# Performance work log

Measured on AMD Instinct MI355X. Metric: run time of the kernel, lower is better.

## Reference

```python
import jax, jax.numpy as jnp
import numpy as np

K = 10           # polynomial order
N = 100000       # num nodes
E = 3200000      # num edges
F_IN = 512       # input feature dim
C = 64           # num classes


def setup_inputs() -> dict:
    key = jax.random.key(0)
    ks = jax.random.split(key, 6)
    x = jax.random.normal(ks[0], (N, F_IN), dtype=jnp.float32)
    edge_index = jax.random.randint(ks[1], (2, E), 0, N, dtype=jnp.int64)
    W = jax.random.normal(ks[2], (F_IN, C), dtype=jnp.float32) * (1.0 / np.sqrt(F_IN))
    b = jax.random.normal(ks[3], (C,), dtype=jnp.float32) * 0.01
    lap_coefs = jax.random.uniform(ks[4], (K + 1,), dtype=jnp.float32)
    mf_weights = jax.random.uniform(ks[5], (1, K + 1, C), dtype=jnp.float32)
    return {"x": x, "edge_index": edge_index, "W": W, "b": b,
            "lap_coefs": lap_coefs, "mf_weights": mf_weights}


def reference(x, edge_index, W, b, lap_coefs, mf_weights):
    row, col = edge_index[0], edge_index[1]
    # GCN norm without self-loops: deg over targets (col), sym normalization
    ones = jnp.ones((row.shape[0],), dtype=x.dtype)
    deg = jax.ops.segment_sum(ones, col, num_segments=N)
    dinv = jnp.where(deg > 0, jax.lax.rsqrt(jnp.maximum(deg, 1.0)), 1.0)
    norm = dinv[row] * dinv[col]  # [E]

    h = x @ W + b  # [N, C]  (dropout is identity in eval mode)

    def prop(hx):
        # out[i] = sum_{(j->i)} norm_e * hx[j]
        return jax.ops.segment_sum(norm[:, None] * hx[row], col, num_segments=N)

    outs = [h, prop(h)]
    for _ in range(2, K + 1):
        # P_n = Bn*P_{n-1} + Cn*P_{n-2} + An*prop(P_{n-1}), An=2, Bn=0, Cn=-1
        outs.append(2.0 * prop(outs[-1]) - outs[-2])

    # coef_upd='none' -> coefs used directly; P0 gets coef 1, P_i gets lap_coefs[i-1]
    coefs = jnp.concatenate([jnp.ones((1,), lap_coefs.dtype), lap_coefs[:K]])  # [K+1]
    stacked = jnp.stack(outs, axis=1)  # [N, K+1, C]
    ret = jnp.sum(stacked * coefs[None, :, None] * mf_weights, axis=1)  # [N, C]
    return jax.nn.log_softmax(ret, axis=-1)
```

## Files before the change

kernel.cpp:

```cpp
#include <hip/hip_runtime.h>

#define F_IN 512
#define C_DIM 64
#define BUCKET_BITS 9
#define EPB 2048

typedef __bf16 bf16x8 __attribute__((ext_vector_type(8)));
typedef float f32x4 __attribute__((ext_vector_type(4)));

__device__ inline unsigned bf_rne(float x) {
    unsigned u = __float_as_uint(x);
    u += 0x7fffu + ((u >> 16) & 1u);
    return u >> 16;
}
__device__ inline unsigned bfpack(float x, float y) {
    return bf_rne(x) | (bf_rne(y) << 16);
}
__device__ inline bf16x8 as_bf16x8(uint4 u) {
    bf16x8 v; __builtin_memcpy(&v, &u, 16); return v;
}

__global__ void deg_kernel(const int* __restrict__ col, int* __restrict__ deg, int E) {
    int i = blockIdx.x * blockDim.x + threadIdx.x;
    int e = i * 4;
    if (e + 3 < E) {
        int4 c4 = *(const int4*)(col + e);
        atomicAdd(&deg[c4.x], 1);
        atomicAdd(&deg[c4.y], 1);
        atomicAdd(&deg[c4.z], 1);
        atomicAdd(&deg[c4.w], 1);
    } else if (e < E) {
        for (int j = e; j < E; ++j) atomicAdd(&deg[col[j]], 1);
    }
}

__global__ void dinv_kernel(const int* __restrict__ deg, float* __restrict__ dinv, int N) {
    int i = blockIdx.x * blockDim.x + threadIdx.x;
    if (i < N) {
        int d = deg[i];
        dinv[i] = (d > 0) ? (1.0f / sqrtf((float)d)) : 1.0f;
    }
}

__global__ void scan1(const int* __restrict__ deg, int* __restrict__ rowptr,
                      int* __restrict__ bsum, int N) {
    __shared__ int tmp[1024];
    int t = threadIdx.x;
    int gid = blockIdx.x * 1024 + t;
    int v = (gid < N) ? deg[gid] : 0;
    tmp[t] = v;
    __syncthreads();
    for (int off = 1; off < 1024; off <<= 1) {
        int u = (t >= off) ? tmp[t - off] : 0;
        __syncthreads();
        tmp[t] += u;
        __syncthreads();
    }
    if (gid < N) rowptr[gid] = tmp[t] - v;
    if (t == 1023) bsum[blockIdx.x] = tmp[1023];
}

__global__ void scan2(int* __restrict__ bs, int nb) {
    __shared__ int tmp[1024];
    int t = threadIdx.x;
    int v = (t < nb) ? bs[t] : 0;
    tmp[t] = v;
    __syncthreads();
    for (int off = 1; off < 1024; off <<= 1) {
        int u = (t >= off) ? tmp[t - off] : 0;
        __syncthreads();
        tmp[t] += u;
        __syncthreads();
    }
    if (t < nb) bs[t] = tmp[t] - v;
}

__global__ void scan3(int* __restrict__ rowptr, const int* __restrict__ bs, int E, int N) {
    int gid = blockIdx.x * 1024 + threadIdx.x;
    if (gid < N) rowptr[gid] += bs[blockIdx.x];
    if (gid == 0) rowptr[N] = E;
}

__global__ void bucketptr_kernel(const int* __restrict__ rowptr, int* __restrict__ bucketptr,
                                 int N, int NB) {
    int b = blockIdx.x * blockDim.x + threadIdx.x;
    if (b <= NB) {
        int idx = b << BUCKET_BITS;
        if (idx > N) idx = N;
        bucketptr[b] = rowptr[idx];
    }
}

__global__ void bucket_scatter(const int* __restrict__ row, const int* __restrict__ col,
                               const float* __restrict__ dinv,
                               const int* __restrict__ bucketptr, int* __restrict__ bcnt,
                               int2* __restrict__ staged, int* __restrict__ staged_dst, int E) {
    __shared__ int lcnt[256];
    __shared__ int lbase[256];
    int t = threadIdx.x;
    lcnt[t] = 0;
    __syncthreads();
    int base_e = blockIdx.x * EPB;
    int rr[8], cc[8], pk[8];
    #pragma unroll
    for (int j = 0; j < 8; ++j) {
        int e = base_e + j * 256 + t;
        pk[j] = -1;
        if (e < E) {
            rr[j] = row[e];
            cc[j] = col[e];
            int b = cc[j] >> BUCKET_BITS;
            int off = atomicAdd(&lcnt[b], 1);
            pk[j] = off | (b << 20);
        }
    }
    __syncthreads();
    lbase[t] = atomicAdd(&bcnt[t], lcnt[t]);
    __syncthreads();
    #pragma unroll
    for (int j = 0; j < 8; ++j) {
        if (pk[j] >= 0) {
            int b = pk[j] >> 20;
            int off = pk[j] & 0xFFFFF;
            int pos = bucketptr[b] + lbase[b] + off;
            staged[pos] = make_int2(rr[j], __float_as_int(dinv[rr[j]] * dinv[cc[j]]));
            staged_dst[pos] = cc[j];
        }
    }
}

__global__ void final_scatter(const int2* __restrict__ staged, const int* __restrict__ staged_dst,
                              const int* __restrict__ rowptr, int* __restrict__ cnt,
                              int2* __restrict__ edges, int E) {
    int i = blockIdx.x * blockDim.x + threadIdx.x;
    if (i >= E) return;
    int c = staged_dst[i];
    int pos = rowptr[c] + atomicAdd(&cnt[c], 1);
    edges[pos] = staged[i];
}

__global__ void wprep_kernel(const float* __restrict__ W,
                             uint4* __restrict__ whi, uint4* __restrict__ wlo) {
    int tid = blockIdx.x * 256 + threadIdx.x;
    int kslot = tid >> 8;
    int rem = tid & 255;
    int ct = rem >> 6;
    int l = rem & 63;
    int col = ct * 16 + (l & 15);
    int kbase = kslot * 32 + ((l >> 4) << 3);
    unsigned hbits[8], lbits[8];
    #pragma unroll
    for (int j = 0; j < 8; ++j) {
        float f = W[(size_t)(kbase + j) * C_DIM + col];
        unsigned h = bf_rne(f);
        hbits[j] = h;
        lbits[j] = bf_rne(f - __uint_as_float(h << 16));
    }
    whi[tid] = make_uint4(hbits[0] | (hbits[1] << 16), hbits[2] | (hbits[3] << 16),
                          hbits[4] | (hbits[5] << 16), hbits[6] | (hbits[7] << 16));
    wlo[tid] = make_uint4(lbits[0] | (lbits[1] << 16), lbits[2] | (lbits[3] << 16),
                          lbits[4] | (lbits[5] << 16), lbits[6] | (lbits[7] << 16));
}

__global__ __launch_bounds__(256) void gemm_mfma(const float4* __restrict__ x4,
                                                 const uint4* __restrict__ whi,
                                                 const uint4* __restrict__ wlo,
                                                 const float* __restrict__ bias,
                                                 uint4* __restrict__ hb, int N) {
    __shared__ float smem[8704];
    char* ahi = (char*)smem;
    char* alo = ahi + 16384;
    const int t = threadIdx.x;
    const int l = t & 63;
    const int wv = t >> 6;
    const int rowblk = blockIdx.x * 128;

    f32x4 acc[2][4];
    #pragma unroll
    for (int rt = 0; rt < 2; ++rt)
        #pragma unroll
        for (int ct = 0; ct < 4; ++ct) acc[rt][ct] = (f32x4){0.f, 0.f, 0.f, 0.f};

    for (int chunk = 0; chunk < 8; ++chunk) {
        #pragma unroll
        for (int i = 0; i < 4; ++i) {
            int idx = t + 256 * i;
            int r = idx >> 3, g = idx & 7;
            int grow = rowblk + r;
            float4 v0 = make_float4(0.f, 0.f, 0.f, 0.f), v1 = v0;
            if (grow < N) {
                const float4* p = x4 + (size_t)grow * (F_IN / 4) + chunk * 16 + g * 2;
                v0 = p[0]; v1 = p[1];
            }
            float f[8] = {v0.x, v0.y, v0.z, v0.w, v1.x, v1.y, v1.z, v1.w};
            unsigned hbits[8], lbits[8];
            #pragma unroll
            for (int j = 0; j < 8; ++j) {
                unsigned h = bf_rne(f[j]);
                hbits[j] = h;
                lbits[j] = bf_rne(f[j] - __uint_as_float(h << 16));
            }
            int off = r * 128 + ((g ^ (r & 7)) << 4);
            *(uint4*)(ahi + off) = make_uint4(hbits[0] | (hbits[1] << 16), hbits[2] | (hbits[3] << 16),
                                              hbits[4] | (hbits[5] << 16), hbits[6] | (hbits[7] << 16));
            *(uint4*)(alo + off) = make_uint4(lbits[0] | (lbits[1] << 16), lbits[2] | (lbits[3] << 16),
                                              lbits[4] | (lbits[5] << 16), lbits[6] | (lbits[7] << 16));
        }
        __syncthreads();
        uint4 AH[2][2], AL[2][2];
        #pragma unroll
        for (int rt = 0; rt < 2; ++rt) {
            int r = wv * 32 + rt * 16 + (l & 15);
            int rb = r * 128;
            int rx = r & 7;
            #pragma unroll
            for (int ks = 0; ks < 2; ++ks) {
                int gl = ks * 4 + (l >> 4);
                int off = rb + ((gl ^ rx) << 4);
                AH[rt][ks] = *(const uint4*)(ahi + off);
                AL[rt][ks] = *(const uint4*)(alo + off);
            }
        }
        #pragma unroll
        for (int ct = 0; ct < 4; ++ct) {
            int base = (chunk * 8 + ct) * 64 + l;
            uint4 BH0 = whi[base], BH1 = whi[base + 256];
            uint4 BL0 = wlo[base], BL1 = wlo[base + 256];
            #pragma unroll
            for (int rt = 0; rt < 2; ++rt) {
                f32x4 c = acc[rt][ct];
                c = __builtin_amdgcn_mfma_f32_16x16x32_bf16(as_bf16x8(AH[rt][0]), as_bf16x8(BH0), c, 0, 0, 0);
                c = __builtin_amdgcn_mfma_f32_16x16x32_bf16(as_bf16x8(AH[rt][1]), as_bf16x8(BH1), c, 0, 0, 0);
                c = __builtin_amdgcn_mfma_f32_16x16x32_bf16(as_bf16x8(AL[rt][0]), as_bf16x8(BH0), c, 0, 0, 0);
                c = __builtin_amdgcn_mfma_f32_16x16x32_bf16(as_bf16x8(AL[rt][1]), as_bf16x8(BH1), c, 0, 0, 0);
                c = __builtin_amdgcn_mfma_f32_16x16x32_bf16(as_bf16x8(AH[rt][0]), as_bf16x8(BL0), c, 0, 0, 0);
                c = __builtin_amdgcn_mfma_f32_16x16x32_bf16(as_bf16x8(AH[rt][1]), as_bf16x8(BL1), c, 0, 0, 0);
                acc[rt][ct] = c;
            }
        }
        __syncthreads();
    }
    float* ls = smem;
    #pragma unroll
    for (int rt = 0; rt < 2; ++rt) {
        int rbase = wv * 32 + rt * 16 + ((l >> 4) << 2);
        #pragma unroll
        for (int ct = 0; ct < 4; ++ct) {
            int col = ct * 16 + (l & 15);
            float bb = bias[col];
            #pragma unroll
            for (int q = 0; q < 4; ++q)
                ls[(rbase + q) * 68 + col] = acc[rt][ct][q] + bb;
        }
    }
    __syncthreads();
    #pragma unroll
    for (int i = 0; i < 4; ++i) {
        int idx = t + 256 * i;
        int r = idx >> 3, lc = idx & 7;
        int grow = rowblk + r;
        if (grow < N) {
            const float* p = ls + r * 68 + lc * 8;
            float4 A = *(const float4*)p;
            float4 Bv = *(const float4*)(p + 4);
            uint4 nb;
            nb.x = bfpack(A.x, A.y);
            nb.y = bfpack(A.z, A.w);
            nb.z = bfpack(Bv.x, Bv.y);
            nb.w = bfpack(Bv.z, Bv.w);
            hb[(size_t)grow * 8 + lc] = nb;
        }
    }
}

__global__ void prop_kernel(const int* __restrict__ rowptr, const int2* __restrict__ edges,
                            const uint4* __restrict__ Hb, const uint4* Pold,
                            uint4* Pout, float4* ret, const float* lap,
                            const float4* mf4, int k, int mode, int N) {
    int gtid = blockIdx.x * blockDim.x + threadIdx.x;
    int node = gtid >> 3;
    int lc = gtid & 7;
    if (node >= N) return;
    int beg = rowptr[node];
    int end = rowptr[node + 1];
    float a0 = 0.f, a1 = 0.f, a2 = 0.f, a3 = 0.f, a4 = 0.f, a5 = 0.f, a6 = 0.f, a7 = 0.f;

#define EDGE_FMA(SRC, WB) do { \
        float w_ = __int_as_float(WB); \
        uint4 u_ = Hb[(size_t)(SRC) * 8 + lc]; \
        a0 = fmaf(w_, __uint_as_float(u_.x << 16), a0); \
        a1 = fmaf(w_, __uint_as_float(u_.x & 0xffff0000u), a1); \
        a2 = fmaf(w_, __uint_as_float(u_.y << 16), a2); \
        a3 = fmaf(w_, __uint_as_float(u_.y & 0xffff0000u), a3); \
        a4 = fmaf(w_, __uint_as_float(u_.z << 16), a4); \
        a5 = fmaf(w_, __uint_as_float(u_.z & 0xffff0000u), a5); \
        a6 = fmaf(w_, __uint_as_float(u_.w << 16), a6); \
        a7 = fmaf(w_, __uint_as_float(u_.w & 0xffff0000u), a7); \
    } while (0)

    int e = beg;
    if ((e & 1) && e < end) {
        int2 d = edges[e];
        EDGE_FMA(d.x, d.y);
        ++e;
    }
    for (; e + 4 <= end; e += 4) {
        int4 p0v = ((const int4*)edges)[e >> 1];
        int4 p1v = ((const int4*)edges)[(e >> 1) + 1];
        EDGE_FMA(p0v.x, p0v.y);
        EDGE_FMA(p0v.z, p0v.w);
        EDGE_FMA(p1v.x, p1v.y);
        EDGE_FMA(p1v.z, p1v.w);
    }
    for (; e < end; ++e) {
        int2 d = edges[e];
        EDGE_FMA(d.x, d.y);
    }
#undef EDGE_FMA

    size_t ib = (size_t)node * 8 + lc;
    float p0, p1, p2, p3, p4, p5, p6, p7;
    if (mode == 0) {
        p0 = a0; p1 = a1; p2 = a2; p3 = a3; p4 = a4; p5 = a5; p6 = a6; p7 = a7;
    } else {
        uint4 ob = Pold[ib];
        p0 = 2.f * a0 - __uint_as_float(ob.x << 16);
        p1 = 2.f * a1 - __uint_as_float(ob.x & 0xffff0000u);
        p2 = 2.f * a2 - __uint_as_float(ob.y << 16);
        p3 = 2.f * a3 - __uint_as_float(ob.y & 0xffff0000u);
        p4 = 2.f * a4 - __uint_as_float(ob.z << 16);
        p5 = 2.f * a5 - __uint_as_float(ob.z & 0xffff0000u);
        p6 = 2.f * a6 - __uint_as_float(ob.w << 16);
        p7 = 2.f * a7 - __uint_as_float(ob.w & 0xffff0000u);
    }
    uint4 nb;
    nb.x = bfpack(p0, p1);
    nb.y = bfpack(p2, p3);
    nb.z = bfpack(p4, p5);
    nb.w = bfpack(p6, p7);
    Pout[ib] = nb;

    if (ret) {
        float lw = lap[k - 1];
        size_t i16 = (size_t)node * 16 + lc * 2;
        float4 m0 = mf4[k * 16 + lc * 2];
        float4 m1 = mf4[k * 16 + lc * 2 + 1];
        float4 r0 = ret[i16];
        float4 r1 = ret[i16 + 1];
        r0.x = fmaf(lw * m0.x, p0, r0.x);
        r0.y = fmaf(lw * m0.y, p1, r0.y);
        r0.z = fmaf(lw * m0.z, p2, r0.z);
        r0.w = fmaf(lw * m0.w, p3, r0.w);
        r1.x = fmaf(lw * m1.x, p4, r1.x);
        r1.y = fmaf(lw * m1.y, p5, r1.y);
        r1.z = fmaf(lw * m1.z, p6, r1.z);
        r1.w = fmaf(lw * m1.w, p7, r1.w);
        ret[i16] = r0;
        ret[i16 + 1] = r1;
    }
}

__global__ void combine_kernel(const uint4* __restrict__ hb, const uint4* __restrict__ Pall,
                               const float* __restrict__ lap, const float* __restrict__ mf,
                               float4* __restrict__ ret, int Kp, int N) {
    __shared__ float smf[1024];
    __shared__ float slap[32];
    int t = threadIdx.x;
    int nmf = (Kp + 1) * 64;
    for (int i = t; i < nmf; i += 256) smf[i] = mf[i];
    if (t < Kp) slap[t] = lap[t];
    __syncthreads();
    int g = blockIdx.x * 256 + t;
    int node = g >> 3, lc = g & 7;
    if (node >= N) return;
    size_t off = (size_t)node * 8 + lc;
    uint4 u = hb[off];
    const float* m0 = smf + lc * 8;
    float a0 = __uint_as_float(u.x << 16) * m0[0];
    float a1 = __uint_as_float(u.x & 0xffff0000u) * m0[1];
    float a2 = __uint_as_float(u.y << 16) * m0[2];
    float a3 = __uint_as_float(u.y & 0xffff0000u) * m0[3];
    float a4 = __uint_as_float(u.z << 16) * m0[4];
    float a5 = __uint_as_float(u.z & 0xffff0000u) * m0[5];
    float a6 = __uint_as_float(u.w << 16) * m0[6];
    float a7 = __uint_as_float(u.w & 0xffff0000u) * m0[7];
    size_t stride = (size_t)N * 8;
    for (int k = 1; k <= Kp; ++k) {
        uint4 p = Pall[(size_t)(k - 1) * stride + off];
        float cw = slap[k - 1];
        const float* mk = smf + k * 64 + lc * 8;
        a0 = fmaf(cw * mk[0], __uint_as_float(p.x << 16), a0);
        a1 = fmaf(cw * mk[1], __uint_as_float(p.x & 0xffff0000u), a1);
        a2 = fmaf(cw * mk[2], __uint_as_float(p.y << 16), a2);
        a3 = fmaf(cw * mk[3], __uint_as_float(p.y & 0xffff0000u), a3);
        a4 = fmaf(cw * mk[4], __uint_as_float(p.z << 16), a4);
        a5 = fmaf(cw * mk[5], __uint_as_float(p.z & 0xffff0000u), a5);
        a6 = fmaf(cw * mk[6], __uint_as_float(p.w << 16), a6);
        a7 = fmaf(cw * mk[7], __uint_as_float(p.w & 0xffff0000u), a7);
    }
    float m = fmaxf(fmaxf(fmaxf(a0, a1), fmaxf(a2, a3)), fmaxf(fmaxf(a4, a5), fmaxf(a6, a7)));
    for (int o = 1; o < 8; o <<= 1) m = fmaxf(m, __shfl_xor(m, o, 8));
    float s = __expf(a0 - m) + __expf(a1 - m) + __expf(a2 - m) + __expf(a3 - m)
            + __expf(a4 - m) + __expf(a5 - m) + __expf(a6 - m) + __expf(a7 - m);
    for (int o = 1; o < 8; o <<= 1) s += __shfl_xor(s, o, 8);
    float lg = logf(s) + m;
    ret[(size_t)node * 16 + lc * 2]     = make_float4(a0 - lg, a1 - lg, a2 - lg, a3 - lg);
    ret[(size_t)node * 16 + lc * 2 + 1] = make_float4(a4 - lg, a5 - lg, a6 - lg, a7 - lg);
}

__global__ void p0ret_kernel(const uint4* __restrict__ hb, float4* __restrict__ ret,
                             const float4* __restrict__ mf4, int N) {
    int g = blockIdx.x * 256 + threadIdx.x;
    int node = g >> 3, lc = g & 7;
    if (node >= N) return;
    uint4 u = hb[(size_t)node * 8 + lc];
    float4 m0 = mf4[lc * 2], m1 = mf4[lc * 2 + 1];
    float4 r0 = make_float4(__uint_as_float(u.x << 16) * m0.x,
                            __uint_as_float(u.x & 0xffff0000u) * m0.y,
                            __uint_as_float(u.y << 16) * m0.z,
                            __uint_as_float(u.y & 0xffff0000u) * m0.w);
    float4 r1 = make_float4(__uint_as_float(u.z << 16) * m1.x,
                            __uint_as_float(u.z & 0xffff0000u) * m1.y,
                            __uint_as_float(u.w << 16) * m1.z,
                            __uint_as_float(u.w & 0xffff0000u) * m1.w);
    ret[(size_t)node * 16 + lc * 2] = r0;
    ret[(size_t)node * 16 + lc * 2 + 1] = r1;
}

__global__ void lsm_kernel(float* __restrict__ ret, int N) {
    int wid = (blockIdx.x * blockDim.x + threadIdx.x) >> 6;
    int c = threadIdx.x & 63;
    if (wid >= N) return;
    size_t idx = (size_t)wid * C_DIM + c;
    float v = ret[idx];
    float m = v;
    for (int off = 32; off; off >>= 1) m = fmaxf(m, __shfl_xor(m, off, 64));
    float ex = __expf(v - m);
    float s = ex;
    for (int off = 32; off; off >>= 1) s += __shfl_xor(s, off, 64);
    ret[idx] = (v - m) - logf(s);
}

extern "C" void kernel_launch(void* const* d_in, const int* in_sizes, int n_in,
                              void* d_out, int out_size, void* d_ws, size_t ws_size,
                              hipStream_t stream) {
    const float* x   = (const float*)d_in[0];
    const int*   ei  = (const int*)d_in[1];
    const float* W   = (const float*)d_in[2];
    const float* b   = (const float*)d_in[3];
    const float* lap = (const float*)d_in[4];
    const float* mf  = (const float*)d_in[5];
    float* ret = (float*)d_out;

    const int C = in_sizes[3];
    const int FIN = in_sizes[2] / C;
    const int N = in_sizes[0] / FIN;
    const int E = in_sizes[1] / 2;
    const int K = in_sizes[4] - 1;
    const int* rowi = ei;
    const int* coli = ei + E;
    const int NB = (N + (1 << BUCKET_BITS) - 1) >> BUCKET_BITS;

    char* w = (char*)d_ws;
    auto alloc = [&](size_t bytes) {
        void* p = (void*)w;
        w += (bytes + 255) & ~(size_t)255;
        return p;
    };
    int*   deg    = (int*)alloc((size_t)N * 4);
    int*   cnt    = (int*)alloc((size_t)N * 4);
    int*   rowptr = (int*)alloc((size_t)(N + 1) * 4);
    int*   bsum   = (int*)alloc(4096);
    float* dinv   = (float*)alloc((size_t)N * 4);
    int*   bcnt   = (int*)alloc(1024);
    int*   bucketptr = (int*)alloc(4096);
    uint4* whi    = (uint4*)alloc(65536);
    uint4* wlo    = (uint4*)alloc(65536);
    int2*  edges  = (int2*)alloc((size_t)E * 8);
    uint4* hb     = (uint4*)alloc((size_t)N * 128);

    const size_t slab = (size_t)N * 128;
    size_t used = (size_t)(w - (char*)d_ws);
    bool lazy = (ws_size > used) && ((ws_size - used) >= (size_t)K * slab);

    uint4* Pall = nullptr;
    uint4* pb = nullptr;
    int2* staged;
    int* staged_dst;
    if (lazy) {
        Pall = (uint4*)alloc((size_t)K * slab);
        staged = (int2*)Pall;
        staged_dst = (int*)((char*)Pall + (size_t)E * 8);
    } else {
        pb = (uint4*)alloc(slab);
        staged = (int2*)hb;
        staged_dst = (int*)alloc((size_t)E * 4);
    }

    hipMemsetAsync(deg, 0, (size_t)N * 4, stream);
    hipMemsetAsync(cnt, 0, (size_t)N * 4, stream);
    hipMemsetAsync(bcnt, 0, 1024, stream);

    deg_kernel<<<((E + 3) / 4 + 255) / 256, 256, 0, stream>>>(coli, deg, E);
    dinv_kernel<<<(N + 255) / 256, 256, 0, stream>>>(deg, dinv, N);

    int nb = (N + 1023) / 1024;
    scan1<<<nb, 1024, 0, stream>>>(deg, rowptr, bsum, N);
    scan2<<<1, 1024, 0, stream>>>(bsum, nb);
    scan3<<<nb, 1024, 0, stream>>>(rowptr, bsum, E, N);
    bucketptr_kernel<<<(NB + 1 + 255) / 256, 256, 0, stream>>>(rowptr, bucketptr, N, NB);

    bucket_scatter<<<(E + EPB - 1) / EPB, 256, 0, stream>>>(rowi, coli, dinv, bucketptr,
                                                            bcnt, staged, staged_dst, E);
    final_scatter<<<(E + 255) / 256, 256, 0, stream>>>(staged, staged_dst, rowptr, cnt,
                                                       edges, E);

    wprep_kernel<<<16, 256, 0, stream>>>(W, whi, wlo);
    gemm_mfma<<<(N + 127) / 128, 256, 0, stream>>>((const float4*)x, whi, wlo, b, hb, N);

    int pgrid = (N * 8 + 255) / 256;
    if (lazy) {
        prop_kernel<<<pgrid, 256, 0, stream>>>(rowptr, edges, hb, Pall, Pall,
                                               nullptr, nullptr, nullptr, 1, 0, N);
        for (int k2 = 2; k2 <= K; ++k2) {
            const uint4* src  = Pall + (size_t)(k2 - 2) * N * 8;
            const uint4* pold = (k2 == 2) ? hb : Pall + (size_t)(k2 - 3) * N * 8;
            uint4* out = Pall + (size_t)(k2 - 1) * N * 8;
            prop_kernel<<<pgrid, 256, 0, stream>>>(rowptr, edges, src, pold, out,
                                                   nullptr, nullptr, nullptr, k2, 1, N);
        }
        combine_kernel<<<pgrid, 256, 0, stream>>>(hb, Pall, lap, mf, (float4*)ret, K, N);
    } else {
        p0ret_kernel<<<pgrid, 256, 0, stream>>>(hb, (float4*)ret, (const float4*)mf, N);
        prop_kernel<<<pgrid, 256, 0, stream>>>(rowptr, edges, hb, pb, pb, (float4*)ret,
                                               lap, (const float4*)mf, 1, 0, N);
        uint4* gat = pb;
        uint4* st  = hb;
        for (int k2 = 2; k2 <= K; ++k2) {
            prop_kernel<<<pgrid, 256, 0, stream>>>(rowptr, edges, gat, st, st, (float4*)ret,
                                                   lap, (const float4*)mf, k2, 1, N);
            uint4* t2 = gat; gat = st; st = t2;
        }
        lsm_kernel<<<((size_t)N * 64 + 255) / 256, 256, 0, stream>>>(ret, N);
    }
}
```

Baseline: 1.222 ms.

## Build CSR via bucket-local degree counting and shared-memory final scatter

Replaces the global degree atomics, three-pass node-level scan and global-atomic final scatter with a bucket histogram, a single 256-entry bucket scan, bucket staging, and per-bucket kernels. The per-bucket kernels compute degree, rowptr and dinv in shared memory and place edges using shared-memory atomics. This removes several launches, the N-sized memsets and millions of global atomics during CSR preprocessing. In exchange, each bucket is handled by a single 512-thread block, which may limit parallelism (only about 196 blocks), and the staged buffer is read twice.

Result: faster. 1.040 ms (-14.9%).

```diff
diff --git a/kernel.cpp b/kernel.cpp
--- a/kernel.cpp
+++ b/kernel.cpp
@@ -20,81 +20,49 @@
     bf16x8 v; __builtin_memcpy(&v, &u, 16); return v;
 }
 
-__global__ void deg_kernel(const int* __restrict__ col, int* __restrict__ deg, int E) {
-    int i = blockIdx.x * blockDim.x + threadIdx.x;
-    int e = i * 4;
-    if (e + 3 < E) {
-        int4 c4 = *(const int4*)(col + e);
-        atomicAdd(&deg[c4.x], 1);
-        atomicAdd(&deg[c4.y], 1);
-        atomicAdd(&deg[c4.z], 1);
-        atomicAdd(&deg[c4.w], 1);
-    } else if (e < E) {
-        for (int j = e; j < E; ++j) atomicAdd(&deg[col[j]], 1);
-    }
-}
-
-__global__ void dinv_kernel(const int* __restrict__ deg, float* __restrict__ dinv, int N) {
-    int i = blockIdx.x * blockDim.x + threadIdx.x;
-    if (i < N) {
-        int d = deg[i];
-        dinv[i] = (d > 0) ? (1.0f / sqrtf((float)d)) : 1.0f;
-    }
-}
-
-__global__ void scan1(const int* __restrict__ deg, int* __restrict__ rowptr,
-                      int* __restrict__ bsum, int N) {
-    __shared__ int tmp[1024];
+__global__ void bucket_count(const int* __restrict__ col, int* __restrict__ bkcnt, int E) {
+    __shared__ int h[256];
     int t = threadIdx.x;
-    int gid = blockIdx.x * 1024 + t;
-    int v = (gid < N) ? deg[gid] : 0;
+    h[t] = 0;
+    __syncthreads();
+    int base = blockIdx.x * 4096 + t * 4;
+    #pragma unroll
+    for (int j = 0; j < 4; ++j) {
+        int e = base + j * 1024;
+        if (e + 3 < E) {
+            int4 c4 = *(const int4*)(col + e);
+            atomicAdd(&h[c4.x >> BUCKET_BITS], 1);
+            atomicAdd(&h[c4.y >> BUCKET_BITS], 1);
+            atomicAdd(&h[c4.z >> BUCKET_BITS], 1);
+            atomicAdd(&h[c4.w >> BUCKET_BITS], 1);
+        } else if (e < E) {
+            for (int q = e; q < E; ++q) atomicAdd(&h[col[q] >> BUCKET_BITS], 1);
+        }
+    }
+    __syncthreads();
+    if (h[t]) atomicAdd(&bkcnt[t], h[t]);
+}
+
+__global__ void bucket_scan(const int* __restrict__ bkcnt, int* __restrict__ bucketbase,
+                            int NB, int E) {
+    __shared__ int tmp[256];
+    int t = threadIdx.x;
+    int v = (t < NB) ? bkcnt[t] : 0;
     tmp[t] = v;
     __syncthreads();
-    for (int off = 1; off < 1024; off <<= 1) {
+    for (int off = 1; off < 256; off <<= 1) {
         int u = (t >= off) ? tmp[t - off] : 0;
         __syncthreads();
         tmp[t] += u;
         __syncthreads();
     }
-    if (gid < N) rowptr[gid] = tmp[t] - v;
-    if (t == 1023) bsum[blockIdx.x] = tmp[1023];
-}
-
-__global__ void scan2(int* __restrict__ bs, int nb) {
-    __shared__ int tmp[1024];
-    int t = threadIdx.x;
-    int v = (t < nb) ? bs[t] : 0;
-    tmp[t] = v;
-    __syncthreads();
-    for (int off = 1; off < 1024; off <<= 1) {
-        int u = (t >= off) ? tmp[t - off] : 0;
-        __syncthreads();
-        tmp[t] += u;
-        __syncthreads();
-    }
-    if (t < nb) bs[t] = tmp[t] - v;
-}
-
-__global__ void scan3(int* __restrict__ rowptr, const int* __restrict__ bs, int E, int N) {
-    int gid = blockIdx.x * 1024 + threadIdx.x;
-    if (gid < N) rowptr[gid] += bs[blockIdx.x];
-    if (gid == 0) rowptr[N] = E;
-}
-
-__global__ void bucketptr_kernel(const int* __restrict__ rowptr, int* __restrict__ bucketptr,
-                                 int N, int NB) {
-    int b = blockIdx.x * blockDim.x + threadIdx.x;
-    if (b <= NB) {
-        int idx = b << BUCKET_BITS;
-        if (idx > N) idx = N;
-        bucketptr[b] = rowptr[idx];
-    }
-}
-
-__global__ void bucket_scatter(const int* __restrict__ row, const int* __restrict__ col,
-                               const float* __restrict__ dinv,
-                               const int* __restrict__ bucketptr, int* __restrict__ bcnt,
-                               int2* __restrict__ staged, int* __restrict__ staged_dst, int E) {
+    if (t < NB) bucketbase[t] = tmp[t] - v;
+    if (t == 0) bucketbase[NB] = E;
+}
+
+__global__ void bucket_stage(const int* __restrict__ row, const int* __restrict__ col,
+                             const int* __restrict__ bucketbase, int* __restrict__ bcnt2,
+                             int2* __restrict__ staged, int E) {
     __shared__ int lcnt[256];
     __shared__ int lbase[256];
     int t = threadIdx.x;
@@ -115,28 +83,68 @@
         }
     }
     __syncthreads();
-    lbase[t] = atomicAdd(&bcnt[t], lcnt[t]);
+    lbase[t] = lcnt[t] ? atomicAdd(&bcnt2[t], lcnt[t]) : 0;
     __syncthreads();
     #pragma unroll
     for (int j = 0; j < 8; ++j) {
         if (pk[j] >= 0) {
             int b = pk[j] >> 20;
             int off = pk[j] & 0xFFFFF;
-            int pos = bucketptr[b] + lbase[b] + off;
-            staged[pos] = make_int2(rr[j], __float_as_int(dinv[rr[j]] * dinv[cc[j]]));
-            staged_dst[pos] = cc[j];
-        }
-    }
-}
-
-__global__ void final_scatter(const int2* __restrict__ staged, const int* __restrict__ staged_dst,
-                              const int* __restrict__ rowptr, int* __restrict__ cnt,
-                              int2* __restrict__ edges, int E) {
-    int i = blockIdx.x * blockDim.x + threadIdx.x;
-    if (i >= E) return;
-    int c = staged_dst[i];
-    int pos = rowptr[c] + atomicAdd(&cnt[c], 1);
-    edges[pos] = staged[i];
+            int pos = bucketbase[b] + lbase[b] + off;
+            staged[pos] = make_int2(rr[j], cc[j]);
+        }
+    }
+}
+
+__global__ void bucket_deg(const int2* __restrict__ staged, const int* __restrict__ bucketbase,
+                           int* __restrict__ rowptr, float* __restrict__ dinv, int N, int E) {
+    __shared__ int cnt[512];
+    int t = threadIdx.x;
+    int b = blockIdx.x;
+    int beg = bucketbase[b];
+    int end = bucketbase[b + 1];
+    cnt[t] = 0;
+    __syncthreads();
+    for (int i = beg + t; i < end; i += 512)
+        atomicAdd(&cnt[staged[i].y & 511], 1);
+    __syncthreads();
+    int v = cnt[t];
+    for (int off = 1; off < 512; off <<= 1) {
+        int u = (t >= off) ? cnt[t - off] : 0;
+        __syncthreads();
+        cnt[t] += u;
+        __syncthreads();
+    }
+    int node = (b << BUCKET_BITS) + t;
+    if (node < N) {
+        rowptr[node] = beg + cnt[t] - v;
+        dinv[node] = (v > 0) ? (1.0f / sqrtf((float)v)) : 1.0f;
+    }
+    if (b == 0 && t == 0) rowptr[N] = E;
+}
+
+__global__ void bucket_final(const int2* __restrict__ staged, const int* __restrict__ bucketbase,
+                             const int* __restrict__ rowptr, const float* __restrict__ dinv,
+                             int2* __restrict__ edges, int N) {
+    __shared__ int lcnt[512];
+    __shared__ int lrow[512];
+    __shared__ float ldinv[512];
+    int t = threadIdx.x;
+    int b = blockIdx.x;
+    int beg = bucketbase[b];
+    int end = bucketbase[b + 1];
+    int node = (b << BUCKET_BITS) + t;
+    lcnt[t] = 0;
+    lrow[t] = (node < N) ? rowptr[node] : 0;
+    ldinv[t] = (node < N) ? dinv[node] : 1.0f;
+    __syncthreads();
+    for (int i = beg + t; i < end; i += 512) {
+        int2 rc = staged[i];
+        int cl = rc.y & 511;
+        float nrm = dinv[rc.x] * ldinv[cl];
+        int pos = lrow[cl] + atomicAdd(&lcnt[cl], 1);
+        edges[pos] = make_int2(rc.x, __float_as_int(nrm));
+    }
 }
 
 __global__ void wprep_kernel(const float* __restrict__ W,
@@ -467,13 +475,11 @@
         w += (bytes + 255) & ~(size_t)255;
         return p;
     };
-    int*   deg    = (int*)alloc((size_t)N * 4);
-    int*   cnt    = (int*)alloc((size_t)N * 4);
     int*   rowptr = (int*)alloc((size_t)(N + 1) * 4);
-    int*   bsum   = (int*)alloc(4096);
     float* dinv   = (float*)alloc((size_t)N * 4);
-    int*   bcnt   = (int*)alloc(1024);
-    int*   bucketptr = (int*)alloc(4096);
+    int*   bkcnt  = (int*)alloc(1024);
+    int*   bucketbase = (int*)alloc(4096);
+    int*   bcnt2  = (int*)alloc(1024);
     uint4* whi    = (uint4*)alloc(65536);
     uint4* wlo    = (uint4*)alloc(65536);
     int2*  edges  = (int2*)alloc((size_t)E * 8);
@@ -486,34 +492,23 @@
     uint4* Pall = nullptr;
     uint4* pb = nullptr;
     int2* staged;
-    int* staged_dst;
     if (lazy) {
         Pall = (uint4*)alloc((size_t)K * slab);
         staged = (int2*)Pall;
-        staged_dst = (int*)((char*)Pall + (size_t)E * 8);
     } else {
         pb = (uint4*)alloc(slab);
         staged = (int2*)hb;
-        staged_dst = (int*)alloc((size_t)E * 4);
-    }
-
-    hipMemsetAsync(deg, 0, (size_t)N * 4, stream);
-    hipMemsetAsync(cnt, 0, (size_t)N * 4, stream);
-    hipMemsetAsync(bcnt, 0, 1024, stream);
-
-    deg_kernel<<<((E + 3) / 4 + 255) / 256, 256, 0, stream>>>(coli, deg, E);
-    dinv_kernel<<<(N + 255) / 256, 256, 0, stream>>>(deg, dinv, N);
-
-    int nb = (N + 1023) / 1024;
-    scan1<<<nb, 1024, 0, stream>>>(deg, rowptr, bsum, N);
-    scan2<<<1, 1024, 0, stream>>>(bsum, nb);
-    scan3<<<nb, 1024, 0, stream>>>(rowptr, bsum, E, N);
-    bucketptr_kernel<<<(NB + 1 + 255) / 256, 256, 0, stream>>>(rowptr, bucketptr, N, NB);
-
-    bucket_scatter<<<(E + EPB - 1) / EPB, 256, 0, stream>>>(rowi, coli, dinv, bucketptr,
-                                                            bcnt, staged, staged_dst, E);
-    final_scatter<<<(E + 255) / 256, 256, 0, stream>>>(staged, staged_dst, rowptr, cnt,
-                                                       edges, E);
+    }
+
+    hipMemsetAsync(bkcnt, 0, 1024, stream);
+    hipMemsetAsync(bcnt2, 0, 1024, stream);
+
+    bucket_count<<<(E + 4095) / 4096, 256, 0, stream>>>(coli, bkcnt, E);
+    bucket_scan<<<1, 256, 0, stream>>>(bkcnt, bucketbase, NB, E);
+    bucket_stage<<<(E + EPB - 1) / EPB, 256, 0, stream>>>(rowi, coli, bucketbase, bcnt2,
+                                                          staged, E);
+    bucket_deg<<<NB, 512, 0, stream>>>(staged, bucketbase, rowptr, dinv, N, E);
+    bucket_final<<<NB, 512, 0, stream>>>(staged, bucketbase, rowptr, dinv, edges, N);
 
     wprep_kernel<<<16, 256, 0, stream>>>(W, whi, wlo);
     gemm_mfma<<<(N + 127) / 128, 256, 0, stream>>>((const float4*)x, whi, wlo, b, hb, N);
```
